# Performance work log

Hardware: AMD Instinct MI355X
Metric: run time of the kernel (lower is better)

The kernel has to match this reference:

```python
import jax, jax.numpy as jnp
import numpy as np


def setup_inputs() -> dict:
    key = jax.random.key(0)
    k1, k2 = jax.random.split(key)
    x = jax.random.normal(k1, (4, 2048, 512), dtype=jnp.float32)
    proxy = jax.random.normal(k2, (16, 512), dtype=jnp.float32)
    return {"x": x, "proxy": proxy}


def reference(x, proxy):
    # x: (B, S, D), proxy: (P, D)
    num_proxies = proxy.shape[0]
    # prods: (B, P, S) = proxy @ x^T per batch
    prods = jnp.einsum('pd,bsd->bps', proxy, x)
    # broadcast outer product: (B, P, S, D), then running prefix sum over seq
    y = jnp.cumsum(prods[..., None] * x[:, None, :, :], axis=2)
    # softmax gate over proxies (dim=1), scaled by sqrt(P)
    w = jax.nn.softmax(prods / jnp.sqrt(jnp.float32(num_proxies)), axis=1)
    # weighted sum over proxies -> (B, S, D)
    out = jnp.einsum('bps,bpsd->bsd', w, y)
    return out
```

## Files before the change

kernel.cpp:

```cpp
#include <hip/hip_runtime.h>
#include <hip/hip_bf16.h>

#define B 4
#define S 2048
#define D 512
#define P 16
#define NC 64
#define CL 32

__global__ __launch_bounds__(256) void k_prods(const float* __restrict__ x,
                                               const float* __restrict__ proxy,
                                               float* __restrict__ prods,
                                               float* __restrict__ wgt) {
    int wid  = (blockIdx.x * blockDim.x + threadIdx.x) >> 6;
    int lane = threadIdx.x & 63;
    if (wid >= B * S) return;

    const float* xr = x + (size_t)wid * D + lane * 8;
    float4 xa = *(const float4*)xr;
    float4 xb = *(const float4*)(xr + 4);

    float part[P];
#pragma unroll
    for (int p = 0; p < P; ++p) {
        const float* pr = proxy + p * D + lane * 8;
        float4 pa = *(const float4*)pr;
        float4 pb = *(const float4*)(pr + 4);
        part[p] = xa.x*pa.x + xa.y*pa.y + xa.z*pa.z + xa.w*pa.w
                + xb.x*pb.x + xb.y*pb.y + xb.z*pb.z + xb.w*pb.w;
    }
#pragma unroll
    for (int p = 0; p < P; ++p) {
        float v = part[p];
#pragma unroll
        for (int off = 32; off > 0; off >>= 1) v += __shfl_xor(v, off);
        part[p] = v;
    }
    float m = part[0];
#pragma unroll
    for (int p = 1; p < P; ++p) m = fmaxf(m, part[p]);
    float e[P];
    float den = 0.f;
#pragma unroll
    for (int p = 0; p < P; ++p) { e[p] = __expf((part[p] - m) * 0.25f); den += e[p]; }
    float inv = 1.f / den;

    int lp = lane & 15;
    float myp = part[0], mye = e[0];
#pragma unroll
    for (int p = 1; p < P; ++p) {
        bool sel = (lp == p);
        myp = sel ? part[p] : myp;
        mye = sel ? e[p]    : mye;
    }
    if (lane < P) {
        prods[(size_t)wid * P + lane] = myp;
        wgt  [(size_t)wid * P + lane] = mye * inv;
    }
}

__global__ __launch_bounds__(512) void k_totals(const float* __restrict__ x,
                                                const float* __restrict__ prods,
                                                float* __restrict__ T) {
    int c = blockIdx.x & (NC - 1);
    int b = blockIdx.x >> 6;
    int d = threadIdx.x;

    float acc[P];
#pragma unroll
    for (int p = 0; p < P; ++p) acc[p] = 0.f;

    int bs0 = b * S + c * CL;
#pragma unroll 4
    for (int i = 0; i < CL; ++i) {
        int bs = bs0 + i;
        float xv = x[(size_t)bs * D + d];
        const float4* pp = (const float4*)(prods + (size_t)bs * P);
        float pr[P];
        ((float4*)pr)[0] = pp[0];
        ((float4*)pr)[1] = pp[1];
        ((float4*)pr)[2] = pp[2];
        ((float4*)pr)[3] = pp[3];
#pragma unroll
        for (int p = 0; p < P; ++p) acc[p] = fmaf(pr[p], xv, acc[p]);
    }
    size_t tb = ((size_t)(b * NC + c)) * (P * D) + d;
#pragma unroll
    for (int p = 0; p < P; ++p) T[tb + p * D] = acc[p];
}

__global__ __launch_bounds__(256) void k_scan(float* __restrict__ T) {
    int t = blockIdx.x * blockDim.x + threadIdx.x;
    int d = t & (D - 1);
    int p = (t >> 9) & (P - 1);
    int b = t >> 13;
    size_t base = ((size_t)b * NC * P + p) * D + d;
    float run = 0.f;
#pragma unroll 8
    for (int c = 0; c < NC; ++c) {
        size_t idx = base + (size_t)c * (P * D);
        float v = T[idx];
        T[idx] = run;
        run += v;
    }
}

__global__ __launch_bounds__(512) void k_apply(const float* __restrict__ x,
                                               const float* __restrict__ prods,
                                               const float* __restrict__ wgt,
                                               const float* __restrict__ T,
                                               float* __restrict__ out) {
    int c = blockIdx.x & (NC - 1);
    int b = blockIdx.x >> 6;
    int d = threadIdx.x;

    float st[P];
    size_t tb = ((size_t)(b * NC + c)) * (P * D) + d;
#pragma unroll
    for (int p = 0; p < P; ++p) st[p] = T[tb + p * D];

    int bs0 = b * S + c * CL;
#pragma unroll 2
    for (int i = 0; i < CL; ++i) {
        int bs = bs0 + i;
        float xv = x[(size_t)bs * D + d];
        const float4* pp = (const float4*)(prods + (size_t)bs * P);
        const float4* wp = (const float4*)(wgt   + (size_t)bs * P);
        float pr[P], ww[P];
        ((float4*)pr)[0] = pp[0];
        ((float4*)pr)[1] = pp[1];
        ((float4*)pr)[2] = pp[2];
        ((float4*)pr)[3] = pp[3];
        ((float4*)ww)[0] = wp[0];
        ((float4*)ww)[1] = wp[1];
        ((float4*)ww)[2] = wp[2];
        ((float4*)ww)[3] = wp[3];
        float o = 0.f;
#pragma unroll
        for (int p = 0; p < P; ++p) {
            st[p] = fmaf(pr[p], xv, st[p]);
            o = fmaf(ww[p], st[p], o);
        }
        out[(size_t)bs * D + d] = o;
    }
}

extern "C" void kernel_launch(void* const* d_in, const int* in_sizes, int n_in,
                              void* d_out, int out_size, void* d_ws, size_t ws_size,
                              hipStream_t stream) {
    const float* x     = (const float*)d_in[0];
    const float* proxy = (const float*)d_in[1];
    float* out   = (float*)d_out;

    float* prods = (float*)d_ws;
    float* wgt   = prods + (size_t)B * S * P;
    float* T     = wgt   + (size_t)B * S * P;

    k_prods <<<(B * S) / 4, 256, 0, stream>>>(x, proxy, prods, wgt);
    k_totals<<<B * NC,     512, 0, stream>>>(x, prods, T);
    k_scan  <<<(B * P * D) / 256, 256, 0, stream>>>(T);
    k_apply <<<B * NC,     512, 0, stream>>>(x, prods, wgt, T, out);
}
```

Before: 40.92 us.

## Use transpose-style shuffle reduction, prefetch x rows, batch scan loads, nontemporal stores

Replaces the 16 independent full-wave reductions in k_prods with a butterfly transpose reduction, so each lane ends up holding one proxy's dot product and the softmax is done with lane shuffles. In k_totals and k_apply, all 32 x values of a chunk are loaded up front to raise memory-level parallelism. k_scan loads all 64 chunk totals into registers before writing, and runs with 128-thread blocks. Output stores become nontemporal. Together these cut shuffle count and latency stalls, at the cost of more register pressure.

```diff
diff --git a/kernel.cpp b/kernel.cpp
--- a/kernel.cpp
+++ b/kernel.cpp
@@ -29,33 +29,52 @@
         part[p] = xa.x*pa.x + xa.y*pa.y + xa.z*pa.z + xa.w*pa.w
                 + xb.x*pb.x + xb.y*pb.y + xb.z*pb.z + xb.w*pb.w;
     }
+
+    float a8[8];
 #pragma unroll
-    for (int p = 0; p < P; ++p) {
-        float v = part[p];
+    for (int k = 0; k < 8; ++k) {
+        bool hi = lane & 1;
+        float mine = hi ? part[2*k+1] : part[2*k];
+        float oth  = hi ? part[2*k]   : part[2*k+1];
+        a8[k] = mine + __shfl_xor(oth, 1);
+    }
+    float a4[4];
 #pragma unroll
-        for (int off = 32; off > 0; off >>= 1) v += __shfl_xor(v, off);
-        part[p] = v;
+    for (int k = 0; k < 4; ++k) {
+        bool hi = lane & 2;
+        float mine = hi ? a8[2*k+1] : a8[2*k];
+        float oth  = hi ? a8[2*k]   : a8[2*k+1];
+        a4[k] = mine + __shfl_xor(oth, 2);
     }
-    float m = part[0];
+    float a2[2];
 #pragma unroll
-    for (int p = 1; p < P; ++p) m = fmaxf(m, part[p]);
-    float e[P];
-    float den = 0.f;
+    for (int k = 0; k < 2; ++k) {
+        bool hi = lane & 4;
+        float mine = hi ? a4[2*k+1] : a4[2*k];
+        float oth  = hi ? a4[2*k]   : a4[2*k+1];
+        a2[k] = mine + __shfl_xor(oth, 4);
+    }
+    float a1;
+    {
+        bool hi = lane & 8;
+        float mine = hi ? a2[1] : a2[0];
+        float oth  = hi ? a2[0] : a2[1];
+        a1 = mine + __shfl_xor(oth, 8);
+    }
+    a1 += __shfl_xor(a1, 16);
+    a1 += __shfl_xor(a1, 32);
+
+    float m = a1;
 #pragma unroll
-    for (int p = 0; p < P; ++p) { e[p] = __expf((part[p] - m) * 0.25f); den += e[p]; }
-    float inv = 1.f / den;
+    for (int off = 1; off < 16; off <<= 1) m = fmaxf(m, __shfl_xor(m, off));
+    float e = __expf((a1 - m) * 0.25f);
+    float den = e;
+#pragma unroll
+    for (int off = 1; off < 16; off <<= 1) den += __shfl_xor(den, off);
 
-    int lp = lane & 15;
-    float myp = part[0], mye = e[0];
-#pragma unroll
-    for (int p = 1; p < P; ++p) {
-        bool sel = (lp == p);
-        myp = sel ? part[p] : myp;
-        mye = sel ? e[p]    : mye;
-    }
     if (lane < P) {
-        prods[(size_t)wid * P + lane] = myp;
-        wgt  [(size_t)wid * P + lane] = mye * inv;
+        prods[(size_t)wid * P + lane] = a1;
+        wgt  [(size_t)wid * P + lane] = e / den;
     }
 }
 
@@ -65,43 +84,48 @@
     int c = blockIdx.x & (NC - 1);
     int b = blockIdx.x >> 6;
     int d = threadIdx.x;
+    int bs0 = b * S + c * CL;
+
+    float xv[CL];
+#pragma unroll
+    for (int i = 0; i < CL; ++i) xv[i] = x[(size_t)(bs0 + i) * D + d];
 
     float acc[P];
 #pragma unroll
     for (int p = 0; p < P; ++p) acc[p] = 0.f;
 
-    int bs0 = b * S + c * CL;
-#pragma unroll 4
+#pragma unroll
     for (int i = 0; i < CL; ++i) {
-        int bs = bs0 + i;
-        float xv = x[(size_t)bs * D + d];
-        const float4* pp = (const float4*)(prods + (size_t)bs * P);
+        const float4* pp = (const float4*)(prods + (size_t)(bs0 + i) * P);
         float pr[P];
         ((float4*)pr)[0] = pp[0];
         ((float4*)pr)[1] = pp[1];
         ((float4*)pr)[2] = pp[2];
         ((float4*)pr)[3] = pp[3];
 #pragma unroll
-        for (int p = 0; p < P; ++p) acc[p] = fmaf(pr[p], xv, acc[p]);
+        for (int p = 0; p < P; ++p) acc[p] = fmaf(pr[p], xv[i], acc[p]);
     }
     size_t tb = ((size_t)(b * NC + c)) * (P * D) + d;
 #pragma unroll
     for (int p = 0; p < P; ++p) T[tb + p * D] = acc[p];
 }
 
-__global__ __launch_bounds__(256) void k_scan(float* __restrict__ T) {
+__global__ __launch_bounds__(128) void k_scan(float* __restrict__ T) {
     int t = blockIdx.x * blockDim.x + threadIdx.x;
     int d = t & (D - 1);
     int p = (t >> 9) & (P - 1);
     int b = t >> 13;
     size_t base = ((size_t)b * NC * P + p) * D + d;
+
+    float v[NC];
+#pragma unroll
+    for (int c = 0; c < NC; ++c) v[c] = T[base + (size_t)c * (P * D)];
+
     float run = 0.f;
-#pragma unroll 8
+#pragma unroll
     for (int c = 0; c < NC; ++c) {
-        size_t idx = base + (size_t)c * (P * D);
-        float v = T[idx];
-        T[idx] = run;
-        run += v;
+        T[base + (size_t)c * (P * D)] = run;
+        run += v[c];
     }
 }
 
@@ -113,17 +137,20 @@
     int c = blockIdx.x & (NC - 1);
     int b = blockIdx.x >> 6;
     int d = threadIdx.x;
+    int bs0 = b * S + c * CL;
+
+    float xv[CL];
+#pragma unroll
+    for (int i = 0; i < CL; ++i) xv[i] = x[(size_t)(bs0 + i) * D + d];
 
     float st[P];
     size_t tb = ((size_t)(b * NC + c)) * (P * D) + d;
 #pragma unroll
     for (int p = 0; p < P; ++p) st[p] = T[tb + p * D];
 
-    int bs0 = b * S + c * CL;
-#pragma unroll 2
+#pragma unroll
     for (int i = 0; i < CL; ++i) {
-        int bs = bs0 + i;
-        float xv = x[(size_t)bs * D + d];
+        const int bs = bs0 + i;
         const float4* pp = (const float4*)(prods + (size_t)bs * P);
         const float4* wp = (const float4*)(wgt   + (size_t)bs * P);
         float pr[P], ww[P];
@@ -138,10 +165,10 @@
         float o = 0.f;
 #pragma unroll
         for (int p = 0; p < P; ++p) {
-            st[p] = fmaf(pr[p], xv, st[p]);
+            st[p] = fmaf(pr[p], xv[i], st[p]);
             o = fmaf(ww[p], st[p], o);
         }
-        out[(size_t)bs * D + d] = o;
+        __builtin_nontemporal_store(o, &out[(size_t)bs * D + d]);
     }
 }
 
@@ -156,8 +183,8 @@
     float* wgt   = prods + (size_t)B * S * P;
     float* T     = wgt   + (size_t)B * S * P;
 
-    k_prods <<<(B * S) / 4, 256, 0, stream>>>(x, proxy, prods, wgt);
-    k_totals<<<B * NC,     512, 0, stream>>>(x, prods, T);
-    k_scan  <<<(B * P * D) / 256, 256, 0, stream>>>(T);
-    k_apply <<<B * NC,     512, 0, stream>>>(x, prods, wgt, T, out);
+    k_prods <<<(B * S) / 4,        256, 0, stream>>>(x, proxy, prods, wgt);
+    k_totals<<<B * NC,             512, 0, stream>>>(x, prods, T);
+    k_scan  <<<(B * P * D) / 128,  128, 0, stream>>>(T);
+    k_apply <<<B * NC,             512, 0, stream>>>(x, prods, wgt, T, out);
 }
```

Measured after the change: 54.29 us. 32.7% more time.
